# Kernel tuning notes

Measured on AMD Instinct MI355X. Metric: run time of the kernel, lower is better.

The kernel has to match this reference:

```python
import jax, jax.numpy as jnp
import numpy as np

D_MODEL = 1024
N_HEADS = 16
HEAD_DIM = D_MODEL // N_HEADS
D_FF = 4096
EPS = 1e-5


def layer_norm(x, w, b):
    mu = jnp.mean(x, axis=-1, keepdims=True)
    var = jnp.var(x, axis=-1, keepdims=True)
    return (x - mu) * jax.lax.rsqrt(var + EPS) * w + b


def setup_inputs() -> dict:
    key = jax.random.key(0)
    ks = jax.random.split(key, 8)
    B, T, C = 2, 2048, D_MODEL
    s = lambda fan_in: 1.0 / np.sqrt(fan_in)
    return {
        "x": jax.random.normal(ks[0], (B, T, C), dtype=jnp.float32),
        "ln1_w": jnp.ones((C,), jnp.float32),
        "ln1_b": jnp.zeros((C,), jnp.float32),
        "qkv_w": jax.random.normal(ks[1], (3 * C, C), jnp.float32) * s(C),
        "attn_out_w": jax.random.normal(ks[2], (C, C), jnp.float32) * s(C),
        "ln2_w": jnp.ones((C,), jnp.float32),
        "ln2_b": jnp.zeros((C,), jnp.float32),
        "mlp_in_w": jax.random.normal(ks[3], (D_FF, C), jnp.float32) * s(C),
        "mlp_gate_w": jax.random.normal(ks[4], (D_FF, C), jnp.float32) * s(C),
        "mlp_out_w": jax.random.normal(ks[5], (C, D_FF), jnp.float32) * s(D_FF),
    }


def reference(x, ln1_w, ln1_b, qkv_w, attn_out_w, ln2_w, ln2_b,
              mlp_in_w, mlp_gate_w, mlp_out_w):
    B, T, C = x.shape
    # --- causal self-attention (pre-norm) ---
    h = layer_norm(x, ln1_w, ln1_b)
    qkv = h @ qkv_w.T  # [B,T,3C]
    q, k, v = jnp.split(qkv, 3, axis=-1)
    def heads(t):
        return t.reshape(B, T, N_HEADS, HEAD_DIM).transpose(0, 2, 1, 3)  # [B,H,T,Dh]
    q, k, v = heads(q), heads(k), heads(v)
    scale = HEAD_DIM ** -0.5
    scores = jnp.einsum("bhqd,bhkd->bhqk", q, k) * scale  # [B,H,T,T]
    causal = jnp.tril(jnp.ones((T, T), dtype=bool))
    scores = jnp.where(causal, scores, -jnp.inf)
    attn = jax.nn.softmax(scores, axis=-1)
    out = jnp.einsum("bhqk,bhkd->bhqd", attn, v)
    out = out.transpose(0, 2, 1, 3).reshape(B, T, C)
    x = x + out @ attn_out_w.T
    # --- SwiGLU MLP (pre-norm) ---
    h = layer_norm(x, ln2_w, ln2_b)
    acts = jax.nn.silu(h @ mlp_in_w.T) * (h @ mlp_gate_w.T)
    return x + acts @ mlp_out_w.T
```

## Files before the change

kernel.cpp:

```cpp
#include <hip/hip_runtime.h>
#include <cstdint>

typedef unsigned short u16;
typedef __bf16 bf16x8 __attribute__((ext_vector_type(8)));
typedef float  f32x4  __attribute__((ext_vector_type(4)));

struct alignas(16) F4 { float v[4]; };
struct alignas(8)  U4 { u16 v[4]; };
struct alignas(16) U8 { u16 v[8]; };

__device__ __forceinline__ u16 f2bf(float f) {
    union { float f; unsigned int u; } x; x.f = f;
    unsigned int r = x.u + 0x7fffu + ((x.u >> 16) & 1u);
    return (u16)(r >> 16);
}
__device__ __forceinline__ float bf2f(u16 u) {
    union { unsigned int u; float f; } x; x.u = ((unsigned int)u) << 16;
    return x.f;
}
__device__ __forceinline__ f32x4 mfma16(bf16x8 a, bf16x8 b, f32x4 c) {
    return __builtin_amdgcn_mfma_f32_16x16x32_bf16(a, b, c, 0, 0, 0);
}
__device__ __forceinline__ bf16x8 ldf(const u16* p) { return *(const bf16x8*)p; }
__device__ __forceinline__ void gload_lds16(const void* g, void* l) {
    auto* gp = reinterpret_cast<const __attribute__((address_space(1))) unsigned int*>(
        reinterpret_cast<uintptr_t>(g));
    auto* lp = reinterpret_cast<__attribute__((address_space(3))) unsigned int*>(
        reinterpret_cast<uintptr_t>(l));
    __builtin_amdgcn_global_load_lds(gp, lp, 16, 0, 0);
}

__global__ __launch_bounds__(256) void cast_bf16_k(const float* __restrict__ in,
                                                   u16* __restrict__ out, int n4) {
    int i = blockIdx.x * 256 + threadIdx.x;
    if (i >= n4) return;
    F4 v = *(const F4*)(in + (size_t)i * 4);
    U4 o;
    #pragma unroll
    for (int j = 0; j < 4; ++j) o.v[j] = f2bf(v.v[j]);
    *(U4*)(out + (size_t)i * 4) = o;
}

__global__ __launch_bounds__(256) void cast_wig_k(const float* __restrict__ wi,
                                                  const float* __restrict__ wg,
                                                  u16* __restrict__ wig) {
    int i = blockIdx.x * 256 + threadIdx.x;
    const int w  = i >> 7;
    const int c8 = (i & 127) * 8;
    const int f  = ((w >> 6) << 5) | (w & 31);
    const float* src = ((w & 32) ? wg : wi) + (size_t)f * 1024 + c8;
    F4 a = *(const F4*)src;
    F4 b = *(const F4*)(src + 4);
    U8 o;
    #pragma unroll
    for (int j = 0; j < 4; ++j) { o.v[j] = f2bf(a.v[j]); o.v[4 + j] = f2bf(b.v[j]); }
    *(U8*)(wig + (size_t)w * 1024 + c8) = o;
}

__global__ __launch_bounds__(256) void ln_fwd_k(const float* __restrict__ x,
                                                const float* __restrict__ w,
                                                const float* __restrict__ b,
                                                u16* __restrict__ h) {
    const int row = blockIdx.x, tid = threadIdx.x;
    const float* xr = x + (size_t)row * 1024;
    F4 v = *(const F4*)(xr + tid * 4);
    float s  = v.v[0] + v.v[1] + v.v[2] + v.v[3];
    float ss = v.v[0]*v.v[0] + v.v[1]*v.v[1] + v.v[2]*v.v[2] + v.v[3]*v.v[3];
    #pragma unroll
    for (int o = 32; o > 0; o >>= 1) { s += __shfl_down(s, o); ss += __shfl_down(ss, o); }
    __shared__ float red[8];
    const int wave = tid >> 6, lane = tid & 63;
    if (lane == 0) { red[wave] = s; red[4 + wave] = ss; }
    __syncthreads();
    s  = red[0] + red[1] + red[2] + red[3];
    ss = red[4] + red[5] + red[6] + red[7];
    const float mu   = s * (1.0f / 1024.0f);
    const float var  = ss * (1.0f / 1024.0f) - mu * mu;
    const float rstd = rsqrtf(var + 1e-5f);
    U4 o;
    #pragma unroll
    for (int j = 0; j < 4; ++j)
        o.v[j] = f2bf((v.v[j] - mu) * rstd * w[tid * 4 + j] + b[tid * 4 + j]);
    *(U4*)(h + (size_t)row * 1024 + tid * 4) = o;
}

template <int MODE>
__global__ __launch_bounds__(256) void gemm_bt_k(const u16* __restrict__ A,
                                                 const u16* __restrict__ Bm,
                                                 void* __restrict__ Cout,
                                                 const float* __restrict__ resid,
                                                 int M, int N, int K) {
    __shared__ u16 Alds[128 * 32];
    __shared__ u16 Blds[128 * 32];
    const int tid  = threadIdx.x;
    const int lane = tid & 63, wave = tid >> 6;
    const int wr = wave >> 1, wc = wave & 1;
    const int r16 = lane & 15, g16 = lane >> 4;
    const int bn = blockIdx.x, bm = blockIdx.y;

    const int srow = lane >> 2;
    const int scol = (lane & 3) * 8;

    f32x4 acc[4][4] = {};

    for (int k0 = 0; k0 < K; k0 += 32) {
        #pragma unroll
        for (int c = 0; c < 2; ++c) {
            const int ch = wave * 2 + c;
            const u16* ga = A  + ((size_t)bm * 128 + ch * 16 + srow) * K + k0 + scol;
            gload_lds16(ga, &Alds[ch * 512]);
            const u16* gb = Bm + ((size_t)bn * 128 + ch * 16 + srow) * K + k0 + scol;
            gload_lds16(gb, &Blds[ch * 512]);
        }
        __syncthreads();
        bf16x8 af[4], bfr[4];
        #pragma unroll
        for (int m = 0; m < 4; ++m)
            af[m] = *(const bf16x8*)&Alds[(wr * 64 + m * 16 + r16) * 32 + g16 * 8];
        #pragma unroll
        for (int n = 0; n < 4; ++n)
            bfr[n] = *(const bf16x8*)&Blds[(wc * 64 + n * 16 + r16) * 32 + g16 * 8];
        #pragma unroll
        for (int m = 0; m < 4; ++m)
            #pragma unroll
            for (int n = 0; n < 4; ++n)
                acc[m][n] = mfma16(af[m], bfr[n], acc[m][n]);
        __syncthreads();
    }

    #pragma unroll
    for (int m = 0; m < 4; ++m) {
        #pragma unroll
        for (int n = 0; n < 4; ++n) {
            #pragma unroll
            for (int r = 0; r < 4; ++r) {
                const int row = bm * 128 + wr * 64 + m * 16 + g16 * 4 + r;
                const int col = bn * 128 + wc * 64 + n * 16 + r16;
                const float v = acc[m][n][r];
                if (MODE == 0) {
                    ((u16*)Cout)[(size_t)row * N + col] = f2bf(v);
                } else {
                    ((float*)Cout)[(size_t)row * N + col] =
                        resid[(size_t)row * N + col] + v;
                }
            }
        }
    }
}

template <int EPI>
__global__ __launch_bounds__(512, 2)
void gemm256_k(const u16* __restrict__ A, const u16* __restrict__ Bm,
               void* __restrict__ Cout, int lda, int ldb, int kLen,
               int nx, int bnCh, int outLd, int planeEls) {
    __shared__ u16 lds[2][2][2][128 * 64];

    const int tid  = threadIdx.x;
    const int wave = tid >> 6, lane = tid & 63;
    const int wm = wave >> 2, wn = wave & 3;
    const int r16 = lane & 15, g16 = lane >> 4;

    const int cpx = gridDim.x >> 3;
    const int xcd = blockIdx.x & 7, loc = blockIdx.x >> 3;
    const int mCh = cpx / bnCh;
    const int cpr = nx / bnCh;
    const int bm = (xcd / cpr) * mCh + loc / bnCh;
    const int bn = (xcd % cpr) * bnCh + loc % bnCh;
    const int kBeg = blockIdx.z * kLen;
    const int NT = kLen >> 6;

    const int csw = ((lane & 7) ^ (lane >> 3)) * 8;
    const u16* aU = A  + (size_t)(bm * 256) * lda + kBeg;
    const u16* bU = Bm + (size_t)(bn * 256) * ldb + kBeg;
    int aOff[2][2], bOff[2][2];
    #pragma unroll
    for (int h = 0; h < 2; ++h) {
        #pragma unroll
        for (int i = 0; i < 2; ++i) {
            const int wr = wave * 16 + (lane >> 3) + i * 8;
            const int ar = (wr >> 6) * 128 + h * 64 + (wr & 63);
            const int br = (wr >> 5) * 64 + h * 32 + (wr & 31);
            aOff[h][i] = ar * lda + csw;
            bOff[h][i] = br * ldb + csw;
        }
    }

    auto stA = [&](int kt, int h) {
        u16* d = &lds[kt & 1][0][h][wave * 1024];
        gload_lds16(aU + aOff[h][0] + kt * 64, d);
        gload_lds16(aU + aOff[h][1] + kt * 64, d + 512);
    };
    auto stB = [&](int kt, int h) {
        u16* d = &lds[kt & 1][1][h][wave * 1024];
        gload_lds16(bU + bOff[h][0] + kt * 64, d);
        gload_lds16(bU + bOff[h][1] + kt * 64, d + 512);
    };

    int offA[4][2], offB[2][2];
    #pragma unroll
    for (int m = 0; m < 4; ++m)
        #pragma unroll
        for (int ks = 0; ks < 2; ++ks)
            offA[m][ks] = (wm * 64 + m * 16 + r16) * 64 + (((ks * 4 + g16) ^ (r16 & 7)) * 8);
    #pragma unroll
    for (int n = 0; n < 2; ++n)
        #pragma unroll
        for (int ks = 0; ks < 2; ++ks)
            offB[n][ks] = (wn * 32 + n * 16 + r16) * 64 + (((ks * 4 + g16) ^ (r16 & 7)) * 8);

    f32x4 acc[8][4] = {};
    bf16x8 af0[4][2], af1[4][2], b0v[2][2], b1v[2][2];

    auto rdAF0 = [&](int buf) {
        const u16* P = &lds[buf][0][0][0];
        #pragma unroll
        for (int m = 0; m < 4; ++m) {
            af0[m][0] = ldf(P + offA[m][0]);
            af0[m][1] = ldf(P + offA[m][1]);
        }
    };
    auto rdAF1 = [&](int buf) {
        const u16* P = &lds[buf][0][1][0];
        #pragma unroll
        for (int m = 0; m < 4; ++m) {
            af1[m][0] = ldf(P + offA[m][0]);
            af1[m][1] = ldf(P + offA[m][1]);
        }
    };
    auto rdB0 = [&](int buf) {
        const u16* P = &lds[buf][1][0][0];
        #pragma unroll
        for (int n = 0; n < 2; ++n) {
            b0v[n][0] = ldf(P + offB[n][0]);
            b0v[n][1] = ldf(P + offB[n][1]);
        }
    };
    auto rdB1 = [&](int buf) {
        const u16* P = &lds[buf][1][1][0];
        #pragma unroll
        for (int n = 0; n < 2; ++n) {
            b1v[n][0] = ldf(P + offB[n][0]);
            b1v[n][1] = ldf(P + offB[n][1]);
        }
    };

    stA(0, 0); stB(0, 0); stB(0, 1); stA(0, 1);
    stA(1, 0); stB(1, 0); stB(1, 1); stA(1, 1);
    asm volatile("s_waitcnt vmcnt(8)" ::: "memory");
    __builtin_amdgcn_s_barrier();
    rdAF0(0); rdB0(0); rdB1(0); rdAF1(0);

    for (int kt = 0; kt < NT; ++kt) {
        const bool pf = (kt + 2 < NT);
        const int nb = (kt + 1) & 1;

        __builtin_amdgcn_s_setprio(1);
        #pragma unroll
        for (int m = 0; m < 4; ++m)
            #pragma unroll
            for (int n = 0; n < 2; ++n) {
                acc[m][n] = mfma16(af0[m][0], b0v[n][0], acc[m][n]);
                acc[m][n] = mfma16(af0[m][1], b0v[n][1], acc[m][n]);
            }
        __builtin_amdgcn_s_setprio(0);
        __builtin_amdgcn_s_barrier();

        if (pf) { stA(kt + 2, 0); stB(kt + 2, 0); }
        __builtin_amdgcn_s_setprio(1);
        #pragma unroll
        for (int m = 0; m < 4; ++m)
            #pragma unroll
            for (int n = 0; n < 2; ++n) {
                acc[m][n + 2] = mfma16(af0[m][0], b1v[n][0], acc[m][n + 2]);
                acc[m][n + 2] = mfma16(af0[m][1], b1v[n][1], acc[m][n + 2]);
            }
        __builtin_amdgcn_s_setprio(0);
        __builtin_amdgcn_s_barrier();

        if (pf) stB(kt + 2, 1);
        __builtin_amdgcn_s_setprio(1);
        #pragma unroll
        for (int m = 0; m < 4; ++m)
            #pragma unroll
            for (int n = 0; n < 2; ++n) {
                acc[m + 4][n] = mfma16(af1[m][0], b0v[n][0], acc[m + 4][n]);
                acc[m + 4][n] = mfma16(af1[m][1], b0v[n][1], acc[m + 4][n]);
            }
        __builtin_amdgcn_s_setprio(0);
        __builtin_amdgcn_s_barrier();

        if (pf) stA(kt + 2, 1);
        if (pf)               { asm volatile("s_waitcnt vmcnt(8)" ::: "memory"); }
        else if (kt + 1 < NT) { asm volatile("s_waitcnt vmcnt(0)" ::: "memory"); }
        if (kt + 1 < NT) {
            __builtin_amdgcn_s_barrier();
            rdAF0(nb); rdB0(nb);
        }
        __builtin_amdgcn_s_setprio(1);
        #pragma unroll
        for (int m = 0; m < 4; ++m)
            #pragma unroll
            for (int n = 0; n < 2; ++n) {
                acc[m + 4][n + 2] = mfma16(af1[m][0], b1v[n][0], acc[m + 4][n + 2]);
                acc[m + 4][n + 2] = mfma16(af1[m][1], b1v[n][1], acc[m + 4][n + 2]);
            }
        __builtin_amdgcn_s_setprio(0);
        if (kt + 1 < NT) { rdB1(nb); rdAF1(nb); }
    }

    if constexpr (EPI == 1) {
        float* P = (float*)Cout + (size_t)blockIdx.z * planeEls;
        #pragma unroll
        for (int m = 0; m < 8; ++m) {
            #pragma unroll
            for (int n = 0; n < 4; ++n) {
                #pragma unroll
                for (int r = 0; r < 4; ++r) {
                    const int row = bm * 256 + wm * 128 + m * 16 + g16 * 4 + r;
                    const int col = bn * 256 + wn * 64 + n * 16 + r16;
                    P[(size_t)row * outLd + col] = acc[m][n][r];
                }
            }
        }
    } else {
        (void)planeEls;
        u16* O = (u16*)Cout;
        #pragma unroll
        for (int m = 0; m < 8; ++m) {
            #pragma unroll
            for (int n = 0; n < 2; ++n) {
                #pragma unroll
                for (int r = 0; r < 4; ++r) {
                    const int row = bm * 256 + wm * 128 + m * 16 + g16 * 4 + r;
                    const int col = (bn * 4 + wn) * 32 + n * 16 + r16;
                    const float vi = acc[m][n][r];
                    const float vg = acc[m][n + 2][r];
                    const float sl = vi / (1.0f + __expf(-vi));
                    O[(size_t)row * outLd + col] = f2bf(sl * vg);
                }
            }
        }
    }
}

__global__ __launch_bounds__(256) void addreduce4_k(const float* __restrict__ resid,
                                                    const float* __restrict__ p,
                                                    float* __restrict__ out,
                                                    int n4, int planeEls) {
    for (int i = blockIdx.x * 256 + threadIdx.x; i < n4; i += gridDim.x * 256) {
        F4 a = *(const F4*)(resid + (size_t)i * 4);
        F4 b = *(const F4*)(p + (size_t)i * 4);
        F4 c = *(const F4*)(p + (size_t)planeEls + (size_t)i * 4);
        F4 d = *(const F4*)(p + (size_t)2 * planeEls + (size_t)i * 4);
        F4 e = *(const F4*)(p + (size_t)3 * planeEls + (size_t)i * 4);
        F4 o;
        #pragma unroll
        for (int j = 0; j < 4; ++j) o.v[j] = a.v[j] + b.v[j] + c.v[j] + d.v[j] + e.v[j];
        *(F4*)(out + (size_t)i * 4) = o;
    }
}

__global__ __launch_bounds__(256) void attn_fwd_k(const u16* __restrict__ qk,
                                                  const u16* __restrict__ vt,
                                                  u16* __restrict__ Ob) {
    __shared__ u16 Klds[2][64 * 64];
    __shared__ u16 Vlds[2][64 * 64];

    const int tid  = threadIdx.x;
    const int wave = tid >> 6, lane = tid & 63;
    const int r16  = lane & 15, g16 = lane >> 4;

    const int blk = blockIdx.x;
    const int xcd = blk & 7;
    const int pc  = blk >> 3;
    const int hh  = pc >> 5;
    const int qb  = (31 - (pc & 31) + 8 * hh) & 31;
    const int bh  = xcd * 4 + hh;
    const int h   = bh & 15, b = bh >> 4;

    const int q0w = qb * 64 + wave * 16;
    const size_t seqb = (size_t)b * 2048;

    const u16* qp = qk + (seqb + q0w + r16) * 2048 + h * 64 + g16 * 8;
    const bf16x8 qf0 = *(const bf16x8*)qp;
    const bf16x8 qf1 = *(const bf16x8*)(qp + 32);

    const u16* kbase = qk + seqb * 2048 + 1024 + (size_t)h * 64;
    const u16* vbase = vt + (size_t)(h * 64) * 4096 + seqb;

    const int srow  = tid >> 3;
    const int scol8 = ((tid & 7) ^ (srow & 7)) * 8;
    const u16* ksrc = kbase + (size_t)srow * 2048 + scol8;
    const u16* vsrc = vbase + (size_t)srow * 4096 + scol8;

    auto stage = [&](int bufi, int kv0) {
        const u16* kp = ksrc + (size_t)kv0 * 2048;
        const u16* vp = vsrc + kv0;
        u16* kd = &Klds[bufi][wave * 512];
        u16* vd = &Vlds[bufi][wave * 512];
        gload_lds16(kp, kd);
        gload_lds16(kp + (size_t)32 * 2048, kd + 2048);
        gload_lds16(vp, vd);
        gload_lds16(vp + (size_t)32 * 4096, vd + 2048);
    };

    f32x4 o[4] = {};
    float mreg = -3.0e38f, lreg = 0.0f;
    constexpr float SC = 0.125f * 1.44269504088896341f;

    const int nt = qb + 1;
    stage(0, 0);
    asm volatile("s_waitcnt vmcnt(0)" ::: "memory");
    __builtin_amdgcn_s_barrier();

    for (int it = 0; it < nt; ++it) {
        const int kv0 = it * 64;
        const int cur = it & 1;
        if (it + 1 < nt) stage(cur ^ 1, kv0 + 64);

        const u16* K = Klds[cur];
        const u16* V = Vlds[cur];

        f32x4 s[4];
        #pragma unroll
        for (int t = 0; t < 4; ++t) {
            const int row = 16 * t + r16;
            const int sw  = row & 7;
            const bf16x8 k0 = *(const bf16x8*)&K[row * 64 + ((g16 ^ sw) * 8)];
            const bf16x8 k1 = *(const bf16x8*)&K[row * 64 + (((g16 + 4) ^ sw) * 8)];
            f32x4 acc = {0.f, 0.f, 0.f, 0.f};
            acc = mfma16(k0, qf0, acc);
            acc = mfma16(k1, qf1, acc);
            s[t] = acc;
        }

        float a[16];
        #pragma unroll
        for (int t = 0; t < 4; ++t)
            #pragma unroll
            for (int r = 0; r < 4; ++r) a[4 * t + r] = s[t][r] * SC;

        if (kv0 + 63 > q0w) {
            const int qg = q0w + r16;
            #pragma unroll
            for (int t = 0; t < 4; ++t)
                #pragma unroll
                for (int r = 0; r < 4; ++r)
                    if (kv0 + 16 * t + 4 * g16 + r > qg) a[4 * t + r] = -1.0e30f;
        }

        float mx = a[0];
        #pragma unroll
        for (int j = 1; j < 16; ++j) mx = fmaxf(mx, a[j]);
        mx = fmaxf(mx, __shfl_xor(mx, 16));
        mx = fmaxf(mx, __shfl_xor(mx, 32));
        const float mn = fmaxf(mreg, mx);
        const float al = exp2f(mreg - mn);
        float p[16], rs = 0.0f;
        #pragma unroll
        for (int j = 0; j < 16; ++j) { p[j] = exp2f(a[j] - mn); rs += p[j]; }
        rs += __shfl_xor(rs, 16);
        rs += __shfl_xor(rs, 32);
        lreg = lreg * al + rs;
        mreg = mn;

        bf16x8 pf0, pf1;
        #pragma unroll
        for (int j = 0; j < 8; ++j) { pf0[j] = (__bf16)p[j]; pf1[j] = (__bf16)p[8 + j]; }

        #pragma unroll
        for (int t = 0; t < 4; ++t) {
            const int row  = 16 * t + r16;
            const int sw   = row & 7;
            const int base = row * 64 + (g16 & 1) * 4;
            const int c0   = g16 >> 1;
            U4 a0 = *(const U4*)&V[base + (((c0 + 0) ^ sw) * 8)];
            U4 a1 = *(const U4*)&V[base + (((c0 + 2) ^ sw) * 8)];
            U4 b0 = *(const U4*)&V[base + (((c0 + 4) ^ sw) * 8)];
            U4 b1 = *(const U4*)&V[base + (((c0 + 6) ^ sw) * 8)];
            #pragma unroll
            for (int r = 0; r < 4; ++r) o[t][r] *= al;
            bf16x8 v0, v1;
            #pragma unroll
            for (int j = 0; j < 4; ++j) {
                v0[j]     = ((const __bf16*)&a0)[j];
                v0[4 + j] = ((const __bf16*)&a1)[j];
                v1[j]     = ((const __bf16*)&b0)[j];
                v1[4 + j] = ((const __bf16*)&b1)[j];
            }
            o[t] = mfma16(v0, pf0, o[t]);
            o[t] = mfma16(v1, pf1, o[t]);
        }

        if (it + 1 < nt) {
            asm volatile("s_waitcnt vmcnt(0)" ::: "memory");
            __builtin_amdgcn_s_barrier();
        }
    }

    const float inv = 1.0f / lreg;
    u16* op = Ob + (seqb + q0w + r16) * 1024 + h * 64 + 4 * g16;
    #pragma unroll
    for (int t = 0; t < 4; ++t) {
        U4 st;
        #pragma unroll
        for (int r = 0; r < 4; ++r) st.v[r] = f2bf(o[t][r] * inv);
        *(U4*)(op + 16 * t) = st;
    }
}

extern "C" void kernel_launch(void* const* d_in, const int* in_sizes, int n_in,
                              void* d_out, int out_size, void* d_ws, size_t ws_size,
                              hipStream_t stream) {
    (void)in_sizes; (void)n_in; (void)out_size; (void)ws_size;
    constexpr int C = 1024, FF = 4096, M = 2 * 2048;
    constexpr size_t MB = 1024 * 1024;

    const float* x      = (const float*)d_in[0];
    const float* ln1_w  = (const float*)d_in[1];
    const float* ln1_b  = (const float*)d_in[2];
    const float* qkv_w  = (const float*)d_in[3];
    const float* atto_w = (const float*)d_in[4];
    const float* ln2_w  = (const float*)d_in[5];
    const float* ln2_b  = (const float*)d_in[6];
    const float* mlpi_w = (const float*)d_in[7];
    const float* mlpg_w = (const float*)d_in[8];
    const float* mlpo_w = (const float*)d_in[9];
    float* out = (float*)d_out;

    char* ws = (char*)d_ws;
    size_t off = 0;
    auto alloc = [&](size_t bytes) {
        char* p = ws + off;
        off += (bytes + 255) & ~(size_t)255;
        return p;
    };
    u16*   wq   = (u16*)  alloc((size_t)3 * C * C * 2);
    u16*   wo   = (u16*)  alloc((size_t)C * C * 2);
    u16*   wig  = (u16*)  alloc((size_t)2 * FF * C * 2);
    u16*   wm   = (u16*)  alloc((size_t)C * FF * 2);
    float* x1   = (float*)alloc((size_t)M * C * 4);
    u16*   h2   = (u16*)  alloc((size_t)M * C * 2);
    u16*   ab   = (u16*)  alloc((size_t)M * FF * 2);
    char*  R    = alloc(64 * MB);
    u16*   h1   = (u16*)R;
    u16*   qk_b = (u16*)(R + 8 * MB);
    u16*   vt_b = (u16*)(R + 24 * MB);
    u16*   Ob   = (u16*)(R + 32 * MB);
    float* pscr = (float*)R;

    cast_bf16_k<<<(3 * C * C / 4) / 256, 256, 0, stream>>>(qkv_w, wq, 3 * C * C / 4);
    cast_bf16_k<<<(C * C / 4) / 256, 256, 0, stream>>>(atto_w, wo, C * C / 4);
    cast_bf16_k<<<(C * FF / 4) / 256, 256, 0, stream>>>(mlpo_w, wm, C * FF / 4);
    cast_wig_k<<<(2 * FF * C / 8) / 256, 256, 0, stream>>>(mlpi_w, mlpg_w, wig);

    ln_fwd_k<<<M, 256, 0, stream>>>(x, ln1_w, ln1_b, h1);
    gemm_bt_k<0><<<dim3(2 * C / 128, M / 128), 256, 0, stream>>>(h1, wq, qk_b, nullptr, M, 2 * C, C);
    const u16* wv = wq + (size_t)2 * C * C;
    gemm_bt_k<0><<<dim3(M / 128, C / 128), 256, 0, stream>>>(wv, h1, vt_b, nullptr, C, M, C);
    attn_fwd_k<<<1024, 256, 0, stream>>>(qk_b, vt_b, Ob);
    gemm_bt_k<1><<<dim3(C / 128, M / 128), 256, 0, stream>>>(Ob, wo, x1, x, M, C, C);

    ln_fwd_k<<<M, 256, 0, stream>>>(x1, ln2_w, ln2_b, h2);
    gemm256_k<2><<<dim3((2 * FF / 256) * (M / 256), 1, 1), 512, 0, stream>>>(
        h2, wig, ab, C, C, C, 2 * FF / 256, 8, FF, 0);
    gemm256_k<1><<<dim3((C / 256) * (M / 256), 1, 4), 512, 0, stream>>>(
        ab, wm, pscr, FF, FF, FF / 4, C / 256, 4, C, M * C);
    addreduce4_k<<<2048, 256, 0, stream>>>(x1, pscr, out, M * C / 4, M * C);
}
```

Before: 293.9 us.

## Merge weight casts and QKV GEMMs, split-K attn-out with fused residual+LN, bf16 partials

Replaces four weight-cast launches with one combined cast kernel and merges the QK and V-transposed GEMMs into a single launch. The attention output projection becomes a two-way split-K GEMM writing bf16 partials. A new kernel sums the residual with those partials and applies LayerNorm in the same pass. The MLP-out split-K partials are now stored as bf16 instead of fp32, halving scratch traffic. This cuts launch count and memory bandwidth, but rounding the partial sums to bf16 before the residual add costs precision.

```diff
diff --git a/kernel.cpp b/kernel.cpp
--- a/kernel.cpp
+++ b/kernel.cpp
@@ -30,31 +30,36 @@
     __builtin_amdgcn_global_load_lds(gp, lp, 16, 0, 0);
 }
 
-__global__ __launch_bounds__(256) void cast_bf16_k(const float* __restrict__ in,
-                                                   u16* __restrict__ out, int n4) {
-    int i = blockIdx.x * 256 + threadIdx.x;
-    if (i >= n4) return;
-    F4 v = *(const F4*)(in + (size_t)i * 4);
-    U4 o;
-    #pragma unroll
-    for (int j = 0; j < 4; ++j) o.v[j] = f2bf(v.v[j]);
-    *(U4*)(out + (size_t)i * 4) = o;
-}
-
-__global__ __launch_bounds__(256) void cast_wig_k(const float* __restrict__ wi,
+__global__ __launch_bounds__(256) void cast_all_k(const float* __restrict__ qkvw,
+                                                  const float* __restrict__ attow,
+                                                  const float* __restrict__ mlpow,
+                                                  const float* __restrict__ wi,
                                                   const float* __restrict__ wg,
+                                                  u16* __restrict__ wq,
+                                                  u16* __restrict__ wo,
+                                                  u16* __restrict__ wm,
                                                   u16* __restrict__ wig) {
-    int i = blockIdx.x * 256 + threadIdx.x;
-    const int w  = i >> 7;
-    const int c8 = (i & 127) * 8;
-    const int f  = ((w >> 6) << 5) | (w & 31);
-    const float* src = ((w & 32) ? wg : wi) + (size_t)f * 1024 + c8;
+    constexpr int N1 = 3 * 1024 * 1024 / 8;
+    constexpr int N2 = N1 + 1024 * 1024 / 8;
+    constexpr int N3 = N2 + 1024 * 4096 / 8;
+    const int i = blockIdx.x * 256 + threadIdx.x;
+    const float* src; u16* dst;
+    if (i < N1)      { src = qkvw  + (size_t)i * 8;        dst = wq + (size_t)i * 8; }
+    else if (i < N2) { const int j = i - N1; src = attow + (size_t)j * 8; dst = wo + (size_t)j * 8; }
+    else if (i < N3) { const int j = i - N2; src = mlpow + (size_t)j * 8; dst = wm + (size_t)j * 8; }
+    else {
+        const int j = i - N3;
+        const int w = j >> 7, c8 = (j & 127) * 8;
+        const int f = ((w >> 6) << 5) | (w & 31);
+        src = ((w & 32) ? wg : wi) + (size_t)f * 1024 + c8;
+        dst = wig + (size_t)w * 1024 + c8;
+    }
     F4 a = *(const F4*)src;
     F4 b = *(const F4*)(src + 4);
     U8 o;
     #pragma unroll
     for (int j = 0; j < 4; ++j) { o.v[j] = f2bf(a.v[j]); o.v[4 + j] = f2bf(b.v[j]); }
-    *(U8*)(wig + (size_t)w * 1024 + c8) = o;
+    *(U8*)dst = o;
 }
 
 __global__ __launch_bounds__(256) void ln_fwd_k(const float* __restrict__ x,
@@ -84,19 +89,62 @@
     *(U4*)(h + (size_t)row * 1024 + tid * 4) = o;
 }
 
-template <int MODE>
-__global__ __launch_bounds__(256) void gemm_bt_k(const u16* __restrict__ A,
-                                                 const u16* __restrict__ Bm,
-                                                 void* __restrict__ Cout,
-                                                 const float* __restrict__ resid,
-                                                 int M, int N, int K) {
-    __shared__ u16 Alds[128 * 32];
-    __shared__ u16 Blds[128 * 32];
+__global__ __launch_bounds__(256) void ln_resid_k(const float* __restrict__ x,
+                                                  const u16* __restrict__ p,
+                                                  const float* __restrict__ w,
+                                                  const float* __restrict__ b,
+                                                  float* __restrict__ x1,
+                                                  u16* __restrict__ h,
+                                                  int planeEls) {
+    const int row = blockIdx.x, tid = threadIdx.x;
+    const size_t base = (size_t)row * 1024 + tid * 4;
+    F4 xv = *(const F4*)(x + base);
+    U4 q0 = *(const U4*)(p + base);
+    U4 q1 = *(const U4*)(p + (size_t)planeEls + base);
+    F4 sv;
+    #pragma unroll
+    for (int j = 0; j < 4; ++j) sv.v[j] = xv.v[j] + bf2f(q0.v[j]) + bf2f(q1.v[j]);
+    *(F4*)(x1 + base) = sv;
+    float s  = sv.v[0] + sv.v[1] + sv.v[2] + sv.v[3];
+    float ss = sv.v[0]*sv.v[0] + sv.v[1]*sv.v[1] + sv.v[2]*sv.v[2] + sv.v[3]*sv.v[3];
+    #pragma unroll
+    for (int o = 32; o > 0; o >>= 1) { s += __shfl_down(s, o); ss += __shfl_down(ss, o); }
+    __shared__ float red[8];
+    const int wave = tid >> 6, lane = tid & 63;
+    if (lane == 0) { red[wave] = s; red[4 + wave] = ss; }
+    __syncthreads();
+    s  = red[0] + red[1] + red[2] + red[3];
+    ss = red[4] + red[5] + red[6] + red[7];
+    const float mu   = s * (1.0f / 1024.0f);
+    const float var  = ss * (1.0f / 1024.0f) - mu * mu;
+    const float rstd = rsqrtf(var + 1e-5f);
+    U4 o;
+    #pragma unroll
+    for (int j = 0; j < 4; ++j)
+        o.v[j] = f2bf((sv.v[j] - mu) * rstd * w[tid * 4 + j] + b[tid * 4 + j]);
+    *(U4*)(h + base) = o;
+}
+
+__global__ __launch_bounds__(256) void gemm_qkvt_k(const u16* __restrict__ h1,
+                                                   const u16* __restrict__ wq,
+                                                   u16* __restrict__ qk_b,
+                                                   u16* __restrict__ vt_b) {
+    __shared__ alignas(16) u16 Alds[128 * 32];
+    __shared__ alignas(16) u16 Blds[128 * 32];
     const int tid  = threadIdx.x;
     const int lane = tid & 63, wave = tid >> 6;
     const int wr = wave >> 1, wc = wave & 1;
     const int r16 = lane & 15, g16 = lane >> 4;
-    const int bn = blockIdx.x, bm = blockIdx.y;
+
+    const u16* A; const u16* Bm; u16* Cout; int bn, bm, N;
+    const int bid = blockIdx.x;
+    if (bid < 512) { A = h1; Bm = wq; Cout = qk_b; N = 2048; bn = bid & 15; bm = bid >> 4; }
+    else {
+        const int id = bid - 512;
+        A = wq + (size_t)2 * 1024 * 1024;
+        Bm = h1; Cout = vt_b; N = 4096; bn = id & 31; bm = id >> 5;
+    }
+    constexpr int K = 1024;
 
     const int srow = lane >> 2;
     const int scol = (lane & 3) * 8;
@@ -116,10 +164,10 @@
         bf16x8 af[4], bfr[4];
         #pragma unroll
         for (int m = 0; m < 4; ++m)
-            af[m] = *(const bf16x8*)&Alds[(wr * 64 + m * 16 + r16) * 32 + g16 * 8];
+            af[m] = ldf(&Alds[(wr * 64 + m * 16 + r16) * 32 + g16 * 8]);
         #pragma unroll
         for (int n = 0; n < 4; ++n)
-            bfr[n] = *(const bf16x8*)&Blds[(wc * 64 + n * 16 + r16) * 32 + g16 * 8];
+            bfr[n] = ldf(&Blds[(wc * 64 + n * 16 + r16) * 32 + g16 * 8]);
         #pragma unroll
         for (int m = 0; m < 4; ++m)
             #pragma unroll
@@ -129,23 +177,72 @@
     }
 
     #pragma unroll
-    for (int m = 0; m < 4; ++m) {
-        #pragma unroll
-        for (int n = 0; n < 4; ++n) {
+    for (int m = 0; m < 4; ++m)
+        #pragma unroll
+        for (int n = 0; n < 4; ++n)
             #pragma unroll
             for (int r = 0; r < 4; ++r) {
                 const int row = bm * 128 + wr * 64 + m * 16 + g16 * 4 + r;
                 const int col = bn * 128 + wc * 64 + n * 16 + r16;
-                const float v = acc[m][n][r];
-                if (MODE == 0) {
-                    ((u16*)Cout)[(size_t)row * N + col] = f2bf(v);
-                } else {
-                    ((float*)Cout)[(size_t)row * N + col] =
-                        resid[(size_t)row * N + col] + v;
-                }
+                Cout[(size_t)row * N + col] = f2bf(acc[m][n][r]);
             }
-        }
-    }
+}
+
+__global__ __launch_bounds__(256) void gemm_btsplit_k(const u16* __restrict__ A,
+                                                      const u16* __restrict__ Bm,
+                                                      u16* __restrict__ P,
+                                                      int N, int K, int kchunk,
+                                                      int planeEls) {
+    __shared__ alignas(16) u16 Alds[128 * 32];
+    __shared__ alignas(16) u16 Blds[128 * 32];
+    const int tid  = threadIdx.x;
+    const int lane = tid & 63, wave = tid >> 6;
+    const int wr = wave >> 1, wc = wave & 1;
+    const int r16 = lane & 15, g16 = lane >> 4;
+    const int bn = blockIdx.x, bm = blockIdx.y;
+    const int kBeg = blockIdx.z * kchunk;
+
+    const int srow = lane >> 2;
+    const int scol = (lane & 3) * 8;
+
+    f32x4 acc[4][4] = {};
+
+    for (int k0 = kBeg; k0 < kBeg + kchunk; k0 += 32) {
+        #pragma unroll
+        for (int c = 0; c < 2; ++c) {
+            const int ch = wave * 2 + c;
+            const u16* ga = A  + ((size_t)bm * 128 + ch * 16 + srow) * K + k0 + scol;
+            gload_lds16(ga, &Alds[ch * 512]);
+            const u16* gb = Bm + ((size_t)bn * 128 + ch * 16 + srow) * K + k0 + scol;
+            gload_lds16(gb, &Blds[ch * 512]);
+        }
+        __syncthreads();
+        bf16x8 af[4], bfr[4];
+        #pragma unroll
+        for (int m = 0; m < 4; ++m)
+            af[m] = ldf(&Alds[(wr * 64 + m * 16 + r16) * 32 + g16 * 8]);
+        #pragma unroll
+        for (int n = 0; n < 4; ++n)
+            bfr[n] = ldf(&Blds[(wc * 64 + n * 16 + r16) * 32 + g16 * 8]);
+        #pragma unroll
+        for (int m = 0; m < 4; ++m)
+            #pragma unroll
+            for (int n = 0; n < 4; ++n)
+                acc[m][n] = mfma16(af[m], bfr[n], acc[m][n]);
+        __syncthreads();
+    }
+
+    u16* Pp = P + (size_t)blockIdx.z * planeEls;
+    #pragma unroll
+    for (int m = 0; m < 4; ++m)
+        #pragma unroll
+        for (int n = 0; n < 4; ++n)
+            #pragma unroll
+            for (int r = 0; r < 4; ++r) {
+                const int row = bm * 128 + wr * 64 + m * 16 + g16 * 4 + r;
+                const int col = bn * 128 + wc * 64 + n * 16 + r16;
+                Pp[(size_t)row * N + col] = f2bf(acc[m][n][r]);
+            }
 }
 
 template <int EPI>
@@ -153,7 +250,7 @@
 void gemm256_k(const u16* __restrict__ A, const u16* __restrict__ Bm,
                void* __restrict__ Cout, int lda, int ldb, int kLen,
                int nx, int bnCh, int outLd, int planeEls) {
-    __shared__ u16 lds[2][2][2][128 * 64];
+    __shared__ alignas(16) u16 lds[2][2][2][128 * 64];
 
     const int tid  = threadIdx.x;
     const int wave = tid >> 6, lane = tid & 63;
@@ -174,7 +271,7 @@
     const u16* bU = Bm + (size_t)(bn * 256) * ldb + kBeg;
     int aOff[2][2], bOff[2][2];
     #pragma unroll
-    for (int h = 0; h < 2; ++h) {
+    for (int h = 0; h < 2; ++h)
         #pragma unroll
         for (int i = 0; i < 2; ++i) {
             const int wr = wave * 16 + (lane >> 3) + i * 8;
@@ -183,7 +280,6 @@
             aOff[h][i] = ar * lda + csw;
             bOff[h][i] = br * ldb + csw;
         }
-    }
 
     auto stA = [&](int kt, int h) {
         u16* d = &lds[kt & 1][0][h][wave * 1024];
@@ -214,34 +310,22 @@
     auto rdAF0 = [&](int buf) {
         const u16* P = &lds[buf][0][0][0];
         #pragma unroll
-        for (int m = 0; m < 4; ++m) {
-            af0[m][0] = ldf(P + offA[m][0]);
-            af0[m][1] = ldf(P + offA[m][1]);
-        }
+        for (int m = 0; m < 4; ++m) { af0[m][0] = ldf(P + offA[m][0]); af0[m][1] = ldf(P + offA[m][1]); }
     };
     auto rdAF1 = [&](int buf) {
         const u16* P = &lds[buf][0][1][0];
         #pragma unroll
-        for (int m = 0; m < 4; ++m) {
-            af1[m][0] = ldf(P + offA[m][0]);
-            af1[m][1] = ldf(P + offA[m][1]);
-        }
+        for (int m = 0; m < 4; ++m) { af1[m][0] = ldf(P + offA[m][0]); af1[m][1] = ldf(P + offA[m][1]); }
     };
     auto rdB0 = [&](int buf) {
         const u16* P = &lds[buf][1][0][0];
         #pragma unroll
-        for (int n = 0; n < 2; ++n) {
-            b0v[n][0] = ldf(P + offB[n][0]);
-            b0v[n][1] = ldf(P + offB[n][1]);
-        }
+        for (int n = 0; n < 2; ++n) { b0v[n][0] = ldf(P + offB[n][0]); b0v[n][1] = ldf(P + offB[n][1]); }
     };
     auto rdB1 = [&](int buf) {
         const u16* P = &lds[buf][1][1][0];
         #pragma unroll
-        for (int n = 0; n < 2; ++n) {
-            b1v[n][0] = ldf(P + offB[n][0]);
-            b1v[n][1] = ldf(P + offB[n][1]);
-        }
+        for (int n = 0; n < 2; ++n) { b1v[n][0] = ldf(P + offB[n][0]); b1v[n][1] = ldf(P + offB[n][1]); }
     };
 
     stA(0, 0); stB(0, 0); stB(0, 1); stA(0, 1);
@@ -309,26 +393,24 @@
     }
 
     if constexpr (EPI == 1) {
-        float* P = (float*)Cout + (size_t)blockIdx.z * planeEls;
-        #pragma unroll
-        for (int m = 0; m < 8; ++m) {
-            #pragma unroll
-            for (int n = 0; n < 4; ++n) {
+        u16* P = (u16*)Cout + (size_t)blockIdx.z * planeEls;
+        #pragma unroll
+        for (int m = 0; m < 8; ++m)
+            #pragma unroll
+            for (int n = 0; n < 4; ++n)
                 #pragma unroll
                 for (int r = 0; r < 4; ++r) {
                     const int row = bm * 256 + wm * 128 + m * 16 + g16 * 4 + r;
                     const int col = bn * 256 + wn * 64 + n * 16 + r16;
-                    P[(size_t)row * outLd + col] = acc[m][n][r];
+                    P[(size_t)row * outLd + col] = f2bf(acc[m][n][r]);
                 }
-            }
-        }
     } else {
         (void)planeEls;
         u16* O = (u16*)Cout;
         #pragma unroll
-        for (int m = 0; m < 8; ++m) {
-            #pragma unroll
-            for (int n = 0; n < 2; ++n) {
+        for (int m = 0; m < 8; ++m)
+            #pragma unroll
+            for (int n = 0; n < 2; ++n)
                 #pragma unroll
                 for (int r = 0; r < 4; ++r) {
                     const int row = bm * 256 + wm * 128 + m * 16 + g16 * 4 + r;
@@ -338,24 +420,23 @@
                     const float sl = vi / (1.0f + __expf(-vi));
                     O[(size_t)row * outLd + col] = f2bf(sl * vg);
                 }
-            }
-        }
     }
 }
 
 __global__ __launch_bounds__(256) void addreduce4_k(const float* __restrict__ resid,
-                                                    const float* __restrict__ p,
+                                                    const u16* __restrict__ p,
                                                     float* __restrict__ out,
                                                     int n4, int planeEls) {
     for (int i = blockIdx.x * 256 + threadIdx.x; i < n4; i += gridDim.x * 256) {
         F4 a = *(const F4*)(resid + (size_t)i * 4);
-        F4 b = *(const F4*)(p + (size_t)i * 4);
-        F4 c = *(const F4*)(p + (size_t)planeEls + (size_t)i * 4);
-        F4 d = *(const F4*)(p + (size_t)2 * planeEls + (size_t)i * 4);
-        F4 e = *(const F4*)(p + (size_t)3 * planeEls + (size_t)i * 4);
+        U4 q0 = *(const U4*)(p + (size_t)i * 4);
+        U4 q1 = *(const U4*)(p + (size_t)planeEls + (size_t)i * 4);
+        U4 q2 = *(const U4*)(p + (size_t)2 * planeEls + (size_t)i * 4);
+        U4 q3 = *(const U4*)(p + (size_t)3 * planeEls + (size_t)i * 4);
         F4 o;
         #pragma unroll
-        for (int j = 0; j < 4; ++j) o.v[j] = a.v[j] + b.v[j] + c.v[j] + d.v[j] + e.v[j];
+        for (int j = 0; j < 4; ++j)
+            o.v[j] = a.v[j] + bf2f(q0.v[j]) + bf2f(q1.v[j]) + bf2f(q2.v[j]) + bf2f(q3.v[j]);
         *(F4*)(out + (size_t)i * 4) = o;
     }
 }
@@ -363,8 +444,8 @@
 __global__ __launch_bounds__(256) void attn_fwd_k(const u16* __restrict__ qk,
                                                   const u16* __restrict__ vt,
                                                   u16* __restrict__ Ob) {
-    __shared__ u16 Klds[2][64 * 64];
-    __shared__ u16 Vlds[2][64 * 64];
+    __shared__ alignas(16) u16 Klds[2][64 * 64];
+    __shared__ alignas(16) u16 Vlds[2][64 * 64];
 
     const int tid  = threadIdx.x;
     const int wave = tid >> 6, lane = tid & 63;
@@ -547,21 +628,19 @@
     u16*   qk_b = (u16*)(R + 8 * MB);
     u16*   vt_b = (u16*)(R + 24 * MB);
     u16*   Ob   = (u16*)(R + 32 * MB);
-    float* pscr = (float*)R;
-
-    cast_bf16_k<<<(3 * C * C / 4) / 256, 256, 0, stream>>>(qkv_w, wq, 3 * C * C / 4);
-    cast_bf16_k<<<(C * C / 4) / 256, 256, 0, stream>>>(atto_w, wo, C * C / 4);
-    cast_bf16_k<<<(C * FF / 4) / 256, 256, 0, stream>>>(mlpo_w, wm, C * FF / 4);
-    cast_wig_k<<<(2 * FF * C / 8) / 256, 256, 0, stream>>>(mlpi_w, mlpg_w, wig);
+    u16*   aoP  = (u16*)(R + 40 * MB);
+    u16*   pscr = (u16*)R;
+
+    cast_all_k<<<8192, 256, 0, stream>>>(qkv_w, atto_w, mlpo_w, mlpi_w, mlpg_w,
+                                         wq, wo, wm, wig);
 
     ln_fwd_k<<<M, 256, 0, stream>>>(x, ln1_w, ln1_b, h1);
-    gemm_bt_k<0><<<dim3(2 * C / 128, M / 128), 256, 0, stream>>>(h1, wq, qk_b, nullptr, M, 2 * C, C);
-    const u16* wv = wq + (size_t)2 * C * C;
-    gemm_bt_k<0><<<dim3(M / 128, C / 128), 256, 0, stream>>>(wv, h1, vt_b, nullptr, C, M, C);
+    gemm_qkvt_k<<<768, 256, 0, stream>>>(h1, wq, qk_b, vt_b);
     attn_fwd_k<<<1024, 256, 0, stream>>>(qk_b, vt_b, Ob);
-    gemm_bt_k<1><<<dim3(C / 128, M / 128), 256, 0, stream>>>(Ob, wo, x1, x, M, C, C);
-
-    ln_fwd_k<<<M, 256, 0, stream>>>(x1, ln2_w, ln2_b, h2);
+    gemm_btsplit_k<<<dim3(C / 128, M / 128, 2), 256, 0, stream>>>(
+        Ob, wo, aoP, C, C, C / 2, M * C);
+    ln_resid_k<<<M, 256, 0, stream>>>(x, aoP, ln2_w, ln2_b, x1, h2, M * C);
+
     gemm256_k<2><<<dim3((2 * FF / 256) * (M / 256), 1, 1), 512, 0, stream>>>(
         h2, wig, ab, C, C, C, 2 * FF / 256, 8, FF, 0);
     gemm256_k<1><<<dim3((C / 256) * (M / 256), 1, 4), 512, 0, stream>>>(
```

New measurement: 256.6 us. 1.15x faster.
